# Kernel tuning notes

Measured on AMD Instinct MI355X. Metric: run time of the kernel, lower is better.

The kernel has to match this reference:

```python
import jax, jax.numpy as jnp
import numpy as np

N = 50000
E = 800000
IN_C, HID_C, OUT_C = 512, 256, 64
K = 10
ALPHA = 0.1


def setup_inputs() -> dict:
    key = jax.random.key(0)
    k1, k2, k3, k4, k5, k6 = jax.random.split(key, 6)
    x = jax.random.normal(k1, (N, IN_C), dtype=jnp.float32)
    edge_index = jax.random.randint(k2, (2, E), 0, N, dtype=jnp.int64)
    # Linear params (torch nn.Linear: y = x @ W.T + b), kaiming-ish scale
    W1 = jax.random.normal(k3, (HID_C, IN_C), dtype=jnp.float32) / np.sqrt(IN_C)
    b1 = jax.random.normal(k4, (HID_C,), dtype=jnp.float32) * 0.01
    W2 = jax.random.normal(k5, (OUT_C, HID_C), dtype=jnp.float32) / np.sqrt(HID_C)
    b2 = jax.random.normal(k6, (OUT_C,), dtype=jnp.float32) * 0.01
    return {"x": x, "edge_index": edge_index, "W1": W1, "b1": b1, "W2": W2, "b2": b2}


def reference(x, edge_index, W1, b1, W2, b2):
    # MLP head (dropout is identity in eval mode)
    h = jax.nn.relu(x @ W1.T + b1)          # [N, HID_C]
    z = h @ W2.T + b2                        # [N, OUT_C]

    src = edge_index[0]                      # message source
    dst = edge_index[1]                      # message target (aggregation index)

    # GCN symmetric normalization with self-loops (PyG APPNP default)
    ones = jnp.ones((E,), dtype=z.dtype)
    deg = jax.ops.segment_sum(ones, dst, num_segments=N) + 1.0  # +1 for self-loop
    dinv = jax.lax.rsqrt(deg)                # deg^{-1/2}
    edge_norm = (dinv[src] * dinv[dst])[:, None]   # [E, 1]
    self_norm = (dinv * dinv)[:, None]             # [N, 1] self-loop weight

    def step(hcur, _):
        agg = jax.ops.segment_sum(hcur[src] * edge_norm, dst, num_segments=N)
        agg = agg + hcur * self_norm
        hnew = (1.0 - ALPHA) * agg + ALPHA * z
        return hnew, None

    h_final, _ = jax.lax.scan(step, z, None, length=K)
    return h_final
```

## Files before the change

kernel.cpp:

```cpp
#include <hip/hip_runtime.h>

typedef __bf16 bf16x8 __attribute__((ext_vector_type(8)));
typedef float f32x4 __attribute__((ext_vector_type(4)));
typedef short short8 __attribute__((ext_vector_type(8)));

__device__ __forceinline__ unsigned short f2bf_u(float f) {
    unsigned u = __builtin_bit_cast(unsigned, f);
    u += 0x7FFFu + ((u >> 16) & 1u);
    return (unsigned short)(u >> 16);
}
__device__ __forceinline__ float bf2f(unsigned short h) {
    unsigned u = ((unsigned)h) << 16;
    return __builtin_bit_cast(float, u);
}
__device__ __forceinline__ float i2f(int b) { return __builtin_bit_cast(float, b); }

#define GLOAD_LDS16(gsrc, ldst)                                                        \
    __builtin_amdgcn_global_load_lds((const __attribute__((address_space(1))) void*)(gsrc), \
                                     (__attribute__((address_space(3))) void*)(ldst), 16, 0, 0)

__global__ __launch_bounds__(256)
void prep_a(const void* __restrict__ ei, const float* __restrict__ W1,
            const float* __restrict__ W2, int* __restrict__ flag,
            short* __restrict__ W1h, short* __restrict__ W1l,
            short* __restrict__ W2h, short* __restrict__ W2l,
            int* __restrict__ counts, int N) {
    __shared__ int sflag;
    const int tid = threadIdx.x;
    const int gtid = blockIdx.x * 256 + tid;
    const int gsize = gridDim.x * 256;
    if (blockIdx.x == 0) {
        if (tid == 0) sflag = 0;
        __syncthreads();
        unsigned v = 0;
        for (int i = tid * 2 + 1; i < 2048; i += 512) v |= ((const unsigned*)ei)[i];
        if (v) atomicOr(&sflag, 1);
        __syncthreads();
        if (tid == 0) *flag = sflag;
    }
    for (int i = gtid; i < N; i += gsize) counts[i] = 0;
    const int n1 = 256 * 512, n2 = 64 * 256;
    for (int i = gtid; i < n1; i += gsize) {
        float w0 = W1[i];
        unsigned short h = f2bf_u(w0);
        W1h[i] = (short)h;
        W1l[i] = (short)f2bf_u(w0 - bf2f(h));
    }
    for (int i = gtid; i < n2; i += gsize) {
        float w0 = W2[i];
        unsigned short h = f2bf_u(w0);
        W2h[i] = (short)h;
        W2l[i] = (short)f2bf_u(w0 - bf2f(h));
    }
}

__global__ void convert_count_kernel(const void* __restrict__ edges, const int* __restrict__ flag,
                                     int* __restrict__ src, int* __restrict__ dst,
                                     int* __restrict__ counts, int E) {
    int e = blockIdx.x * 256 + threadIdx.x;
    if (e >= E) return;
    int s, d;
    if (*flag) { const int* p = (const int*)edges; s = p[e]; d = p[E + e]; }
    else       { const long long* p = (const long long*)edges; s = (int)p[e]; d = (int)p[E + e]; }
    src[e] = s;
    dst[e] = d;
    atomicAdd(&counts[d], 1);
}

__global__ void bsum_dinv_kernel(const int* __restrict__ counts, float* __restrict__ dinv,
                                 int* __restrict__ bs, int n) {
    __shared__ int sdata[256];
    int i = blockIdx.x * 256 + threadIdx.x;
    int v = (i < n) ? counts[i] : 0;
    if (i < n) dinv[i] = rsqrtf((float)v + 1.0f);
    sdata[threadIdx.x] = (i < n) ? (v + 1) : 0;
    __syncthreads();
    #pragma unroll
    for (int off = 128; off > 0; off >>= 1) {
        if (threadIdx.x < off) sdata[threadIdx.x] += sdata[threadIdx.x + off];
        __syncthreads();
    }
    if (threadIdx.x == 0) bs[blockIdx.x] = sdata[0];
}

__global__ void scanbs_kernel(const int* __restrict__ bs, int* __restrict__ bsoff, int nb) {
    __shared__ int sdata[256];
    int tid = threadIdx.x;
    int v = (tid < nb) ? bs[tid] : 0;
    sdata[tid] = v;
    __syncthreads();
    #pragma unroll
    for (int off = 1; off < 256; off <<= 1) {
        int t = (tid >= off) ? sdata[tid - off] : 0;
        __syncthreads();
        sdata[tid] += t;
        __syncthreads();
    }
    if (tid < nb) bsoff[tid] = sdata[tid] - v;
}

__global__ void scanblock_kernel(const int* __restrict__ counts, const int* __restrict__ bsoff,
                                 const float* __restrict__ dinv,
                                 int* __restrict__ rowptr, int* __restrict__ cursor,
                                 int2* __restrict__ csr, int n) {
    __shared__ int sdata[256];
    int tid = threadIdx.x;
    int i = blockIdx.x * 256 + tid;
    int v = (i < n) ? (counts[i] + 1) : 0;
    sdata[tid] = v;
    __syncthreads();
    #pragma unroll
    for (int off = 1; off < 256; off <<= 1) {
        int t = (tid >= off) ? sdata[tid - off] : 0;
        __syncthreads();
        sdata[tid] += t;
        __syncthreads();
    }
    int excl = bsoff[blockIdx.x] + sdata[tid] - v;
    if (i < n) {
        rowptr[i] = excl;
        float di = dinv[i];
        csr[excl] = make_int2(i, __builtin_bit_cast(int, di * di));
        cursor[i] = excl + 1;
    }
    if (i == n - 1) rowptr[n] = excl + v;
}

__global__ void fill_kernel(const int* __restrict__ src, const int* __restrict__ dst,
                            const float* __restrict__ dinv, int* __restrict__ cursor,
                            int2* __restrict__ csr, int E) {
    int e = blockIdx.x * 256 + threadIdx.x;
    if (e >= E) return;
    int s = src[e], d = dst[e];
    int pos = atomicAdd(&cursor[d], 1);
    float w = dinv[s] * dinv[d];
    csr[pos] = make_int2(s, __builtin_bit_cast(int, w));
}

__global__ __launch_bounds__(512)
void gemm1f_k(const float* __restrict__ x, const short* __restrict__ Bh,
              const short* __restrict__ Bl, const float* __restrict__ bias,
              short* __restrict__ C, int M) {
    extern __shared__ short lds[];
    short* sA  = lds;
    short* sBh = lds + 16384;
    short* sBl = lds + 32768;
    const int KDIM = 512, LDC = 256;
    const int tid = threadIdx.x, lane = tid & 63, wave = tid >> 6;
    const int wr = wave >> 2, wc = wave & 3;
    const int m0 = blockIdx.x * 256;
    const int lr = lane & 15, lk = lane >> 4;
    const int l4r = lane >> 2, l4u = lane & 3;
    const int arow = tid >> 1, ahalf = tid & 1;

    f32x4 acc[8][4];
    #pragma unroll
    for (int mi = 0; mi < 8; ++mi)
        #pragma unroll
        for (int ni = 0; ni < 4; ++ni) acc[mi][ni] = {0.f, 0.f, 0.f, 0.f};

    float4 fa[4];

    auto a_load = [&](int k0) {
        int grow = m0 + arow; if (grow > M - 1) grow = M - 1;
        const float* s = x + (size_t)grow * KDIM + k0 + ahalf * 16;
        fa[0] = ((const float4*)s)[0];
        fa[1] = ((const float4*)s)[1];
        fa[2] = ((const float4*)s)[2];
        fa[3] = ((const float4*)s)[3];
    };
    auto a_write = [&](int buf) {
        short8 s0, s1;
        s0[0] = (short)f2bf_u(fa[0].x); s0[1] = (short)f2bf_u(fa[0].y);
        s0[2] = (short)f2bf_u(fa[0].z); s0[3] = (short)f2bf_u(fa[0].w);
        s0[4] = (short)f2bf_u(fa[1].x); s0[5] = (short)f2bf_u(fa[1].y);
        s0[6] = (short)f2bf_u(fa[1].z); s0[7] = (short)f2bf_u(fa[1].w);
        s1[0] = (short)f2bf_u(fa[2].x); s1[1] = (short)f2bf_u(fa[2].y);
        s1[2] = (short)f2bf_u(fa[2].z); s1[3] = (short)f2bf_u(fa[2].w);
        s1[4] = (short)f2bf_u(fa[3].x); s1[5] = (short)f2bf_u(fa[3].y);
        s1[6] = (short)f2bf_u(fa[3].z); s1[7] = (short)f2bf_u(fa[3].w);
        int b = buf * 8192 + arow * 32;
        *reinterpret_cast<short8*>(&sA[b + (((2 * ahalf)     ^ (arow & 3)) << 3)]) = s0;
        *reinterpret_cast<short8*>(&sA[b + (((2 * ahalf + 1) ^ (arow & 3)) << 3)]) = s1;
    };
    auto b_dma = [&](int buf, int k0) {
        #pragma unroll
        for (int p = 0; p < 2; ++p) {
            int row = p * 128 + wave * 16 + l4r;
            size_t goff = (size_t)row * KDIM + k0 + ((l4u ^ (row & 3)) << 3);
            int db = buf * 8192 + (p * 128 + wave * 16) * 32;
            GLOAD_LDS16(Bh + goff, sBh + db);
            GLOAD_LDS16(Bl + goff, sBl + db);
        }
    };

    a_load(0);
    b_dma(0, 0);
    asm volatile("s_waitcnt vmcnt(0)" ::: "memory");
    a_write(0);
    __syncthreads();

    int cur = 0;
    #pragma unroll 1
    for (int t = 0; t < 16; ++t) {
        const bool pf = (t < 15);
        if (pf) {
            a_load((t + 1) * 32);
            b_dma(cur ^ 1, (t + 1) * 32);
        }
        {
            bf16x8 af[8], bhf[4], blf[4];
            #pragma unroll
            for (int mi = 0; mi < 8; ++mi) {
                int row = wr * 128 + mi * 16 + lr;
                af[mi] = *reinterpret_cast<const bf16x8*>(
                    &sA[cur * 8192 + row * 32 + ((lk ^ (row & 3)) << 3)]);
            }
            #pragma unroll
            for (int ni = 0; ni < 4; ++ni) {
                int row = wc * 64 + ni * 16 + lr;
                int idx = cur * 8192 + row * 32 + ((lk ^ (row & 3)) << 3);
                bhf[ni] = *reinterpret_cast<const bf16x8*>(&sBh[idx]);
                blf[ni] = *reinterpret_cast<const bf16x8*>(&sBl[idx]);
            }
            #pragma unroll
            for (int mi = 0; mi < 8; ++mi)
                #pragma unroll
                for (int ni = 0; ni < 4; ++ni) {
                    acc[mi][ni] = __builtin_amdgcn_mfma_f32_16x16x32_bf16(af[mi], bhf[ni], acc[mi][ni], 0, 0, 0);
                    acc[mi][ni] = __builtin_amdgcn_mfma_f32_16x16x32_bf16(af[mi], blf[ni], acc[mi][ni], 0, 0, 0);
                }
        }
        asm volatile("s_waitcnt vmcnt(0)" ::: "memory");
        if (pf) a_write(cur ^ 1);
        __syncthreads();
        cur ^= 1;
    }

    #pragma unroll
    for (int ni = 0; ni < 4; ++ni) {
        int col = wc * 64 + ni * 16 + lr;
        float bv = bias[col];
        #pragma unroll
        for (int mi = 0; mi < 8; ++mi) {
            #pragma unroll
            for (int r = 0; r < 4; ++r) {
                int row = m0 + wr * 128 + mi * 16 + lk * 4 + r;
                if (row < M) {
                    float v = fmaxf(acc[mi][ni][r] + bv, 0.0f);
                    C[(size_t)row * LDC + col] = (short)f2bf_u(v);
                }
            }
        }
    }
}

template<int KDIM, int LDC, bool AF32, bool RELU>
__device__ __forceinline__
void gemm_tile(const void* __restrict__ Av, const short* __restrict__ Bh,
               const short* __restrict__ Bl, const float* __restrict__ bias,
               short* __restrict__ C, int M, int m0, int n0,
               short* sAp, short* sBp) {
    constexpr int NT = KDIM / 64;
    const int tid  = threadIdx.x;
    const int lane = tid & 63;
    const int wave = tid >> 6;
    const int wr = wave >> 1, wc = wave & 1;
    const int lr = lane & 15;
    const int lk = lane >> 4;
    const int l8r = lane >> 3;
    const int l8u = lane & 7;
    const int tr = tid >> 3;
    const int tk = tid & 7;

    f32x4 acc[2][2];
    #pragma unroll
    for (int mi = 0; mi < 2; ++mi)
        #pragma unroll
        for (int ni = 0; ni < 2; ++ni) acc[mi][ni] = {0.f, 0.f, 0.f, 0.f};

    float4 fa[2][2];

    auto a_load = [&](int k0) {
        #pragma unroll
        for (int p = 0; p < 2; ++p) {
            int row = p * 64 + tr;
            int grow = m0 + row; if (grow > M - 1) grow = M - 1;
            const float* s = (const float*)Av + (size_t)grow * KDIM + k0 + tk * 8;
            fa[p][0] = *reinterpret_cast<const float4*>(s);
            fa[p][1] = *reinterpret_cast<const float4*>(s + 4);
        }
    };
    auto a_write = [&](int buf) {
        #pragma unroll
        for (int p = 0; p < 2; ++p) {
            int row = p * 64 + tr;
            short8 sh;
            sh[0] = (short)f2bf_u(fa[p][0].x); sh[1] = (short)f2bf_u(fa[p][0].y);
            sh[2] = (short)f2bf_u(fa[p][0].z); sh[3] = (short)f2bf_u(fa[p][0].w);
            sh[4] = (short)f2bf_u(fa[p][1].x); sh[5] = (short)f2bf_u(fa[p][1].y);
            sh[6] = (short)f2bf_u(fa[p][1].z); sh[7] = (short)f2bf_u(fa[p][1].w);
            *reinterpret_cast<short8*>(&sAp[buf * 8192 + row * 64 + ((tk ^ (row & 7)) << 3)]) = sh;
        }
    };
    auto a_dma = [&](int buf, int k0) {
        #pragma unroll
        for (int p = 0; p < 2; ++p) {
            int row = p * 64 + wave * 8 + l8r;
            int grow = m0 + row; if (grow > M - 1) grow = M - 1;
            const short* s = (const short*)Av + (size_t)grow * KDIM + k0 + ((l8u ^ (row & 7)) << 3);
            GLOAD_LDS16(s, sAp + buf * 8192 + p * 4096 + wave * 512);
        }
    };
    auto b_dma = [&](int buf, int k0) {
        int row = wave * 8 + l8r;
        size_t goff = (size_t)(n0 + row) * KDIM + k0 + ((l8u ^ (row & 7)) << 3);
        GLOAD_LDS16(Bh + goff, sBp + (buf * 2 + 0) * 4096 + wave * 512);
        GLOAD_LDS16(Bl + goff, sBp + (buf * 2 + 1) * 4096 + wave * 512);
    };

    if (AF32) {
        a_load(0);
        b_dma(0, 0);
        asm volatile("s_waitcnt vmcnt(0)" ::: "memory");
        a_write(0);
        __syncthreads();
    } else {
        a_dma(0, 0);
        b_dma(0, 0);
        asm volatile("s_waitcnt vmcnt(0)" ::: "memory");
        __builtin_amdgcn_s_barrier();
        asm volatile("" ::: "memory");
    }

    int cur = 0;
    #pragma unroll 1
    for (int t = 0; t < NT; ++t) {
        const bool pf = (t + 1 < NT);
        if (pf) {
            if (AF32) a_load((t + 1) * 64);
            else      a_dma(cur ^ 1, (t + 1) * 64);
            b_dma(cur ^ 1, (t + 1) * 64);
        }
        #pragma unroll
        for (int ks = 0; ks < 2; ++ks) {
            int kg = ks * 4 + lk;
            bf16x8 af[2], bhf[2], blf[2];
            #pragma unroll
            for (int mi = 0; mi < 2; ++mi) {
                int row = wr * 32 + mi * 16 + lr;
                af[mi] = *reinterpret_cast<const bf16x8*>(
                    &sAp[cur * 8192 + row * 64 + ((kg ^ (row & 7)) << 3)]);
            }
            #pragma unroll
            for (int ni = 0; ni < 2; ++ni) {
                int row = wc * 32 + ni * 16 + lr;
                int idx = row * 64 + ((kg ^ (row & 7)) << 3);
                bhf[ni] = *reinterpret_cast<const bf16x8*>(&sBp[(cur * 2 + 0) * 4096 + idx]);
                blf[ni] = *reinterpret_cast<const bf16x8*>(&sBp[(cur * 2 + 1) * 4096 + idx]);
            }
            #pragma unroll
            for (int mi = 0; mi < 2; ++mi)
                #pragma unroll
                for (int ni = 0; ni < 2; ++ni) {
                    acc[mi][ni] = __builtin_amdgcn_mfma_f32_16x16x32_bf16(af[mi], bhf[ni], acc[mi][ni], 0, 0, 0);
                    acc[mi][ni] = __builtin_amdgcn_mfma_f32_16x16x32_bf16(af[mi], blf[ni], acc[mi][ni], 0, 0, 0);
                }
        }
        asm volatile("s_waitcnt vmcnt(0)" ::: "memory");
        if (AF32) { if (pf) a_write(cur ^ 1); __syncthreads(); }
        else { __builtin_amdgcn_s_barrier(); asm volatile("" ::: "memory"); }
        cur ^= 1;
    }

    #pragma unroll
    for (int ni = 0; ni < 2; ++ni) {
        int col = n0 + wc * 32 + ni * 16 + lr;
        float bv = bias[col];
        #pragma unroll
        for (int mi = 0; mi < 2; ++mi) {
            #pragma unroll
            for (int r = 0; r < 4; ++r) {
                int row = m0 + wr * 32 + mi * 16 + lk * 4 + r;
                if (row < M) {
                    float v = acc[mi][ni][r] + bv;
                    if (RELU) v = fmaxf(v, 0.0f);
                    C[(size_t)row * LDC + col] = (short)f2bf_u(v);
                }
            }
        }
    }
}

__global__ __launch_bounds__(512)
void gemm1_k(const float* __restrict__ x, const short* __restrict__ W1h,
             const short* __restrict__ W1l, const float* __restrict__ b1,
             short* __restrict__ Hbf, int M) {
    __shared__ short sAp[2 * 128 * 64];
    __shared__ short sBp[2 * 2 * 64 * 64];
    int t = blockIdx.x;
    gemm_tile<512, 256, true, true>(x, W1h, W1l, b1, Hbf, M, (t >> 2) * 128, (t & 3) * 64, sAp, sBp);
}

__global__ __launch_bounds__(512)
void gemm2_k(const short* __restrict__ Hbf, const short* __restrict__ W2h,
             const short* __restrict__ W2l, const float* __restrict__ b2,
             short* __restrict__ zbf, int M) {
    __shared__ short sAp[2 * 128 * 64];
    __shared__ short sBp[2 * 2 * 64 * 64];
    gemm_tile<256, 64, false, false>(Hbf, W2h, W2l, b2, zbf, M, blockIdx.x * 128, 0, sAp, sBp);
}

__global__ __launch_bounds__(256)
void prop_step(const unsigned short* __restrict__ hin, const unsigned short* __restrict__ zbf,
               const int* __restrict__ rowptr, const int2* __restrict__ csr,
               void* __restrict__ hout, int outf32, int n) {
    const int lane = threadIdx.x & 63;
    const int nwaves = gridDim.x * 4;
    for (int node = blockIdx.x * 4 + (threadIdx.x >> 6); node < n; node += nwaves) {
        int base = node << 6;
        float acc = 0.0f;
        int e  = __builtin_amdgcn_readfirstlane(rowptr[node]);
        int e1 = __builtin_amdgcn_readfirstlane(rowptr[node + 1]);

        for (; e + 8 <= e1; e += 8) {
            int2 r[8]; unsigned short v[8];
            #pragma unroll
            for (int j = 0; j < 8; ++j) r[j] = csr[e + j];
            #pragma unroll
            for (int j = 0; j < 8; ++j) v[j] = hin[((unsigned)r[j].x << 6) + lane];
            #pragma unroll
            for (int j = 0; j < 8; ++j) acc = fmaf(bf2f(v[j]), i2f(r[j].y), acc);
        }
        for (; e + 4 <= e1; e += 4) {
            int2 r[4]; unsigned short v[4];
            #pragma unroll
            for (int j = 0; j < 4; ++j) r[j] = csr[e + j];
            #pragma unroll
            for (int j = 0; j < 4; ++j) v[j] = hin[((unsigned)r[j].x << 6) + lane];
            #pragma unroll
            for (int j = 0; j < 4; ++j) acc = fmaf(bf2f(v[j]), i2f(r[j].y), acc);
        }
        for (; e < e1; ++e) {
            int2 r = csr[e];
            acc = fmaf(bf2f(hin[((unsigned)r.x << 6) + lane]), i2f(r.y), acc);
        }

        float res = 0.9f * acc + 0.1f * bf2f(zbf[base + lane]);
        if (outf32) ((float*)hout)[base + lane] = res;
        else        ((unsigned short*)hout)[base + lane] = f2bf_u(res);
    }
}

extern "C" void kernel_launch(void* const* d_in, const int* in_sizes, int n_in,
                              void* d_out, int out_size, void* d_ws, size_t ws_size,
                              hipStream_t stream) {
    const float* x  = (const float*)d_in[0];
    const void*  ei = d_in[1];
    const float* W1 = (const float*)d_in[2];
    const float* b1 = (const float*)d_in[3];
    const float* W2 = (const float*)d_in[4];
    const float* b2 = (const float*)d_in[5];
    float* dout = (float*)d_out;

    const int IN_C = 512, HID_C = 256, OUT_C = 64, Ksteps = 10;
    const int N = in_sizes[0] / IN_C;
    const int E = in_sizes[1] / 2;

    char* w = (char*)d_ws;
    auto alloc = [&](size_t bytes) { char* p = w; w += (bytes + 255) & ~(size_t)255; return p; };
    int*   flag    = (int*)  alloc(4);
    int*   src32   = (int*)  alloc((size_t)E * 4);
    int*   dst32   = (int*)  alloc((size_t)E * 4);
    int*   counts  = (int*)  alloc((size_t)N * 4);
    int*   rowptr  = (int*)  alloc((size_t)(N + 1) * 4);
    int*   cursor  = (int*)  alloc((size_t)N * 4);
    float* dinv    = (float*)alloc((size_t)N * 4);
    int2*  csr     = (int2*) alloc((size_t)(E + N) * 8);
    short* W1h     = (short*)alloc((size_t)HID_C * IN_C * 2);
    short* W1l     = (short*)alloc((size_t)HID_C * IN_C * 2);
    short* W2h     = (short*)alloc((size_t)OUT_C * HID_C * 2);
    short* W2l     = (short*)alloc((size_t)OUT_C * HID_C * 2);
    short* Hbf     = (short*)alloc((size_t)N * HID_C * 2);
    unsigned short* zbf = (unsigned short*)alloc((size_t)N * OUT_C * 2);
    unsigned short* hA  = (unsigned short*)alloc((size_t)N * OUT_C * 2);
    unsigned short* hB  = (unsigned short*)alloc((size_t)N * OUT_C * 2);
    int*   bs      = (int*)  alloc(256 * 4);
    int*   bsoff   = (int*)  alloc(256 * 4);

    const int egrid = (E + 255) / 256;
    const int nblk = (N + 255) / 256;

    prep_a<<<512, 256, 0, stream>>>(ei, W1, W2, flag, W1h, W1l, W2h, W2l, counts, N);
    convert_count_kernel<<<egrid, 256, 0, stream>>>(ei, flag, src32, dst32, counts, E);
    bsum_dinv_kernel<<<nblk, 256, 0, stream>>>(counts, dinv, bs, N);
    scanbs_kernel<<<1, 256, 0, stream>>>(bs, bsoff, nblk);
    scanblock_kernel<<<nblk, 256, 0, stream>>>(counts, bsoff, dinv, rowptr, cursor, csr, N);
    fill_kernel<<<egrid, 256, 0, stream>>>(src32, dst32, dinv, cursor, csr, E);

    constexpr int G1_LDS = 98304;
    const int g1grid = (N + 255) / 256;
    bool big = hipFuncSetAttribute((const void*)gemm1f_k,
                                   hipFuncAttributeMaxDynamicSharedMemorySize,
                                   G1_LDS) == hipSuccess;
    if (big) {
        gemm1f_k<<<g1grid, 512, G1_LDS, stream>>>(x, W1h, W1l, b1, Hbf, N);
        if (hipGetLastError() != hipSuccess) big = false;
    }
    if (!big) {
        gemm1_k<<<((N + 127) / 128) * 4, 512, 0, stream>>>(x, W1h, W1l, b1, Hbf, N);
    }
    gemm2_k<<<(N + 127) / 128, 512, 0, stream>>>(Hbf, W2h, W2l, b2, (short*)zbf, N);

    const unsigned short* pin = zbf;
    for (int s = 0; s < Ksteps; ++s) {
        bool last = (s == Ksteps - 1);
        void* out = last ? (void*)dout : ((s & 1) ? (void*)hB : (void*)hA);
        prop_step<<<2048, 256, 0, stream>>>(pin, zbf, rowptr, csr,
                                            out, last ? 1 : 0, N);
        pin = (const unsigned short*)out;
    }
}
```

Baseline: 377.0 us.

## Fuse second MLP GEMM into first GEMM epilogue via LDS-staged hidden tile

The first GEMM kernel now keeps its ReLU hidden tile in LDS, 128 rows at a time with an XOR swizzle, instead of writing it to global memory. Each wave then runs the 256-to-64 second GEMM on that tile with MFMA, reading W2 hi/lo directly from global, and writes the bf16 z output. This removes the separate gemm2 launch and the global write and read of the N x 256 hidden matrix. In exchange the epilogue is longer, adds block syncs, and issues uncached W2 global loads per wave.

```diff
diff --git a/kernel.cpp b/kernel.cpp
--- a/kernel.cpp
+++ b/kernel.cpp
@@ -138,14 +138,16 @@
 }
 
 __global__ __launch_bounds__(512)
-void gemm1f_k(const float* __restrict__ x, const short* __restrict__ Bh,
-              const short* __restrict__ Bl, const float* __restrict__ bias,
-              short* __restrict__ C, int M) {
+void gemm_fused_k(const float* __restrict__ x, const short* __restrict__ Bh,
+                  const short* __restrict__ Bl, const float* __restrict__ bias1,
+                  const short* __restrict__ W2h, const short* __restrict__ W2l,
+                  const float* __restrict__ bias2, unsigned short* __restrict__ zbf,
+                  int M) {
     extern __shared__ short lds[];
     short* sA  = lds;
     short* sBh = lds + 16384;
     short* sBl = lds + 32768;
-    const int KDIM = 512, LDC = 256;
+    const int KDIM = 512;
     const int tid = threadIdx.x, lane = tid & 63, wave = tid >> 6;
     const int wr = wave >> 2, wc = wave & 3;
     const int m0 = blockIdx.x * 256;
@@ -237,21 +239,58 @@
         cur ^= 1;
     }
 
-    #pragma unroll
-    for (int ni = 0; ni < 4; ++ni) {
-        int col = wc * 64 + ni * 16 + lr;
-        float bv = bias[col];
-        #pragma unroll
-        for (int mi = 0; mi < 8; ++mi) {
-            #pragma unroll
-            for (int r = 0; r < 4; ++r) {
-                int row = m0 + wr * 128 + mi * 16 + lk * 4 + r;
-                if (row < M) {
-                    float v = fmaxf(acc[mi][ni][r] + bv, 0.0f);
-                    C[(size_t)row * LDC + col] = (short)f2bf_u(v);
+    short* hbuf = lds;
+    #pragma unroll 1
+    for (int half = 0; half < 2; ++half) {
+        if (wr == half) {
+            #pragma unroll
+            for (int ni = 0; ni < 4; ++ni) {
+                int col = wc * 64 + ni * 16 + lr;
+                float bv = bias1[col];
+                int cu = col >> 3, ce = col & 7;
+                #pragma unroll
+                for (int mi = 0; mi < 8; ++mi) {
+                    #pragma unroll
+                    for (int r = 0; r < 4; ++r) {
+                        int row = mi * 16 + lk * 4 + r;
+                        float v = fmaxf(acc[mi][ni][r] + bv, 0.0f);
+                        hbuf[row * 256 + ((cu ^ (row & 7)) << 3) + ce] = (short)f2bf_u(v);
+                    }
                 }
             }
         }
+        __syncthreads();
+        {
+            f32x4 zacc[4];
+            #pragma unroll
+            for (int ni = 0; ni < 4; ++ni) zacc[ni] = {0.f, 0.f, 0.f, 0.f};
+            int lrow = wave * 16 + lr;
+            #pragma unroll
+            for (int ks = 0; ks < 8; ++ks) {
+                int kcol = ks * 32 + lk * 8;
+                bf16x8 af = *reinterpret_cast<const bf16x8*>(
+                    &hbuf[lrow * 256 + (((kcol >> 3) ^ (lrow & 7)) << 3)]);
+                #pragma unroll
+                for (int ni = 0; ni < 4; ++ni) {
+                    int ocol = ni * 16 + lr;
+                    bf16x8 bh = *reinterpret_cast<const bf16x8*>(W2h + ocol * 256 + kcol);
+                    bf16x8 bl = *reinterpret_cast<const bf16x8*>(W2l + ocol * 256 + kcol);
+                    zacc[ni] = __builtin_amdgcn_mfma_f32_16x16x32_bf16(af, bh, zacc[ni], 0, 0, 0);
+                    zacc[ni] = __builtin_amdgcn_mfma_f32_16x16x32_bf16(af, bl, zacc[ni], 0, 0, 0);
+                }
+            }
+            #pragma unroll
+            for (int ni = 0; ni < 4; ++ni) {
+                int col = ni * 16 + lr;
+                float bv2 = bias2[col];
+                #pragma unroll
+                for (int r = 0; r < 4; ++r) {
+                    int row = m0 + half * 128 + wave * 16 + lk * 4 + r;
+                    if (row < M) zbf[(size_t)row * 64 + col] = f2bf_u(zacc[ni][r] + bv2);
+                }
+            }
+        }
+        __syncthreads();
     }
 }
 
@@ -500,17 +539,17 @@
 
     constexpr int G1_LDS = 98304;
     const int g1grid = (N + 255) / 256;
-    bool big = hipFuncSetAttribute((const void*)gemm1f_k,
+    bool big = hipFuncSetAttribute((const void*)gemm_fused_k,
                                    hipFuncAttributeMaxDynamicSharedMemorySize,
                                    G1_LDS) == hipSuccess;
     if (big) {
-        gemm1f_k<<<g1grid, 512, G1_LDS, stream>>>(x, W1h, W1l, b1, Hbf, N);
+        gemm_fused_k<<<g1grid, 512, G1_LDS, stream>>>(x, W1h, W1l, b1, W2h, W2l, b2, zbf, N);
         if (hipGetLastError() != hipSuccess) big = false;
     }
     if (!big) {
         gemm1_k<<<((N + 127) / 128) * 4, 512, 0, stream>>>(x, W1h, W1l, b1, Hbf, N);
-    }
-    gemm2_k<<<(N + 127) / 128, 512, 0, stream>>>(Hbf, W2h, W2l, b2, (short*)zbf, N);
+        gemm2_k<<<(N + 127) / 128, 512, 0, stream>>>(Hbf, W2h, W2l, b2, (short*)zbf, N);
+    }
 
     const unsigned short* pin = zbf;
     for (int s = 0; s < Ksteps; ++s) {
```

Result: slower. 461.7 us (+22.5%).
